# Kernel tuning notes

Measured on AMD Instinct MI355X. Metric: run time of the kernel, lower is better.

The kernel has to match this reference:

```python
import jax, jax.numpy as jnp
import numpy as np

B, FIELD, H_PREV, H_NEXT = 4096, 128, 128, 256


def setup_inputs() -> dict:
    key = jax.random.key(0)
    k0, k1, k2, k3 = jax.random.split(key, 4)
    x0 = jax.random.normal(k0, (B, FIELD), dtype=jnp.float32)
    x = jax.random.normal(k1, (B, H_PREV), dtype=jnp.float32)
    # Conv1d(1, H_NEXT, kernel=stride=H_PREV*FIELD) weight, reshaped so that
    # flat index k = f*H_PREV + p  ->  W[o, f, p]
    fan_in = H_PREV * FIELD
    bound = 1.0 / np.sqrt(fan_in)
    W = jax.random.uniform(k2, (H_NEXT, FIELD, H_PREV), dtype=jnp.float32, minval=-bound, maxval=bound)
    b = jax.random.uniform(k3, (H_NEXT,), dtype=jnp.float32, minval=-bound, maxval=bound)
    return {"x0": x0, "x": x, "W": W, "b": b}


def reference(x0, x, W, b):
    # outer product x0[b,f]*x[b,p] flattened then full-window conv == bilinear form
    outer = x0[:, :, None] * x[:, None, :]            # [B, FIELD, H_PREV]
    out = jnp.einsum('bfp,ofp->bo', outer, W) + b      # [B, H_NEXT]
    return out[:, :, None]                             # [B, H_NEXT, 1] like Conv1d output
```

## Files before the change

kernel.cpp:

```cpp
#include <hip/hip_runtime.h>


typedef _Float16 f16x8 __attribute__((ext_vector_type(8)));
typedef float    f32x4 __attribute__((ext_vector_type(4)));

#define WS_WT_OFF  0
#define WS_XF_OFF  8388608
#define WS_X0_OFF  9437184
#define WS_NEEDED  10485760

__device__ __forceinline__ void gl_lds16(const void* g, void* l) {
  __builtin_amdgcn_global_load_lds(
      (const __attribute__((address_space(1))) void*)g,
      (__attribute__((address_space(3))) void*)l, 16, 0, 0);
}

#define VMW(N) asm volatile("s_waitcnt vmcnt(" #N ")" ::: "memory")

__global__ __launch_bounds__(256) void prep_kernel(
    const float* __restrict__ x0, const float* __restrict__ x,
    const float* __restrict__ W, _Float16* __restrict__ WT2,
    _Float16* __restrict__ Xf, _Float16* __restrict__ X0T2)
{
  int i = blockIdx.x * 256 + threadIdx.x;
  if (i < 524288) {
    int o = i >> 11, k8 = i & 2047;
    const float* s = W + ((size_t)o << 14) + ((size_t)k8 << 3);
    f16x8 h;
#pragma unroll
    for (int e = 0; e < 8; ++e) h[e] = (_Float16)s[e];
    int ks = k8 >> 2, g = k8 & 3, ob = o >> 6, o6 = o & 63;
    int wv = ks >> 6, r = ks & 63, f = r >> 2, q = r & 3;
    int widx = q * 16 + f;
    *(f16x8*)(WT2 + ((size_t)((ob * 512 + wv * 64 + widx) * 4 + g)) * 512 +
              o6 * 8) = h;
  } else if (i < 589824) {
    int j = i - 524288;
    int r = j >> 4, seg = j & 15;
    const float* s = x + r * 128 + seg * 8;
    f16x8 h;
#pragma unroll
    for (int e = 0; e < 8; ++e) h[e] = (_Float16)s[e];
    int segp = seg ^ (r & 7);
    *(f16x8*)(Xf + r * 128 + segp * 8) = h;
  } else {
    int j = i - 589824;
    int mb = j >> 10, rem = j & 1023;
    int row = rem >> 4, jb = rem & 15;
    f16x8 h;
#pragma unroll
    for (int e = 0; e < 8; ++e)
      h[e] = (_Float16)x0[(size_t)(mb * 64 + row) * 128 + jb * 8 + e];
    *(f16x8*)(X0T2 + (size_t)mb * 8192 + row * 128 + (jb ^ (row & 7)) * 8) = h;
  }
}

__global__ __launch_bounds__(512, 2) void gemm_kernel(
    const _Float16* __restrict__ WT2, const _Float16* __restrict__ Xf,
    const _Float16* __restrict__ X0T2, const float* __restrict__ bias,
    float* __restrict__ out)
{
  __shared__ __align__(16) char smem[139264];

  const int bid = blockIdx.x;
  const int mb  = bid >> 2;
  const int ob  = bid & 3;

  const int t  = threadIdx.x;
  const int l  = t & 63;
  const int wv = t >> 6;
  const int lr = l & 15;
  const int lg = l >> 4;
  const int l16 = l * 16;
  const int swz = lr & 7;
  const int slotbase = wv * 12288;

  const char* wsrc = (const char*)WT2 + ((size_t)(ob * 512 + wv * 64)) * 4096;

  const char* xsb = (const char*)Xf + (size_t)mb * 16384;
  gl_lds16(xsb + 0 * 8192 + t * 16, smem + 98304 + 0 * 8192 + t * 16);
  gl_lds16(xsb + 1 * 8192 + t * 16, smem + 98304 + 1 * 8192 + t * 16);
  const char* x0b = (const char*)X0T2 + (size_t)mb * 16384;
  gl_lds16(x0b + 0 * 8192 + t * 16, smem + 114688 + 0 * 8192 + t * 16);
  gl_lds16(x0b + 1 * 8192 + t * 16, smem + 114688 + 1 * 8192 + t * 16);
#pragma unroll
  for (int w = 0; w < 3; ++w)
#pragma unroll
    for (int i = 0; i < 4; ++i)
      gl_lds16(wsrc + w * 4096 + i * 1024 + l16,
               smem + slotbase + w * 4096 + i * 1024 + l16);
  VMW(8);
  __builtin_amdgcn_s_barrier();

  f32x4 acc[4][4] = {};
  f16x8 xa[4], x0v[4], bwA[4], bwB[4];

#pragma unroll
  for (int m = 0; m < 4; ++m)
    xa[m] = *(const f16x8*)(smem + 98304 + (m * 16 + lr) * 256 +
                            (((0 * 4 + lg) ^ swz) << 4));
#pragma unroll
  for (int m = 0; m < 4; ++m)
    x0v[m] = *(const f16x8*)(smem + 114688 + (m * 16 + lr) * 256 +
                             (((wv * 2 + 0) ^ swz) << 4));
#pragma unroll
  for (int n = 0; n < 4; ++n)
    bwA[n] = *(const f16x8*)(smem + slotbase + 0 * 4096 + lg * 1024 +
                             (n * 16 + lr) * 16);

#define STEP(WI, BUFRD, BUFWR, STG, VMC) { \
    if (STG) { \
      _Pragma("unroll") \
      for (int i = 0; i < 4; ++i) \
        gl_lds16(wsrc + ((WI) + 3) * 4096 + i * 1024 + l16, \
                 smem + slotbase + ((WI) % 3) * 4096 + i * 1024 + l16); \
    } \
    VMW(VMC); \
    if ((WI) < 63) { \
      _Pragma("unroll") \
      for (int n = 0; n < 4; ++n) \
        BUFWR[n] = *(const f16x8*)(smem + slotbase + (((WI) + 1) % 3) * 4096 + \
                                   lg * 1024 + (n * 16 + lr) * 16); \
    } \
    f16x8 av[4]; \
    _Pragma("unroll") \
    for (int m = 0; m < 4; ++m) { \
      _Float16 sh = x0v[m][(WI) & 7]; \
      av[m] = xa[m] * sh; \
    } \
    if ((((WI) + 1) & 15) == 0 && (WI) < 63) { \
      _Pragma("unroll") \
      for (int m = 0; m < 4; ++m) \
        xa[m] = *(const f16x8*)(smem + 98304 + (m * 16 + lr) * 256 + \
                 ((((((WI) + 1) >> 4) * 4 + lg) ^ swz) << 4)); \
    } \
    if ((((WI) + 1) & 7) == 0 && (WI) < 63) { \
      _Pragma("unroll") \
      for (int m = 0; m < 4; ++m) \
        x0v[m] = *(const f16x8*)(smem + 114688 + (m * 16 + lr) * 256 + \
                  (((wv * 2 + ((((WI) + 1) >> 3) & 1)) ^ swz) << 4)); \
    } \
    _Pragma("unroll") \
    for (int m = 0; m < 4; ++m) { \
      _Pragma("unroll") \
      for (int n = 0; n < 4; ++n) \
        acc[m][n] = __builtin_amdgcn_mfma_f32_16x16x32_f16( \
            av[m], BUFRD[n], acc[m][n], 0, 0, 0); \
    } \
  }

#define SE(WI, STG, VMC) STEP(WI, bwA, bwB, STG, VMC)
#define SO(WI, STG, VMC) STEP(WI, bwB, bwA, STG, VMC)

  SE(0,1,8)  SO(1,1,8)  SE(2,1,8)  SO(3,1,8)  SE(4,1,8)  SO(5,1,8)
  SE(6,1,8)  SO(7,1,8)  SE(8,1,8)  SO(9,1,8)  SE(10,1,8) SO(11,1,8)
  SE(12,1,8) SO(13,1,8) SE(14,1,8) SO(15,1,8) SE(16,1,8) SO(17,1,8)
  SE(18,1,8) SO(19,1,8) SE(20,1,8) SO(21,1,8) SE(22,1,8) SO(23,1,8)
  SE(24,1,8) SO(25,1,8) SE(26,1,8) SO(27,1,8) SE(28,1,8) SO(29,1,8)
  SE(30,1,8) SO(31,1,8) SE(32,1,8) SO(33,1,8) SE(34,1,8) SO(35,1,8)
  SE(36,1,8) SO(37,1,8) SE(38,1,8) SO(39,1,8) SE(40,1,8) SO(41,1,8)
  SE(42,1,8) SO(43,1,8) SE(44,1,8) SO(45,1,8) SE(46,1,8) SO(47,1,8)
  SE(48,1,8) SO(49,1,8) SE(50,1,8) SO(51,1,8) SE(52,1,8) SO(53,1,8)
  SE(54,1,8) SO(55,1,8) SE(56,1,8) SO(57,1,8) SE(58,1,8) SO(59,1,8)
  SE(60,1,8) SO(61,0,4) SE(62,0,0) SO(63,0,0)

#undef SE
#undef SO
#undef STEP

  asm volatile("s_waitcnt vmcnt(0) lgkmcnt(0)" ::: "memory");
  __builtin_amdgcn_s_barrier();

#pragma unroll
  for (int m = 0; m < 4; ++m)
#pragma unroll
    for (int n = 0; n < 4; ++n)
      *(f32x4*)(smem + wv * 17408 + (n * 16 + lr) * 272 +
                (m * 16 + lg * 4) * 4) = acc[m][n];

  asm volatile("s_waitcnt lgkmcnt(0)" ::: "memory");
  __builtin_amdgcn_s_barrier();

  {
    const int row = t >> 3, c8 = (t & 7) * 8;
    float v[8];
#pragma unroll
    for (int c = 0; c < 8; ++c) {
      float s = 0.f;
#pragma unroll
      for (int w = 0; w < 8; ++w)
        s += *(const float*)(smem + w * 17408 + (c8 + c) * 272 + row * 4);
      v[c] = s;
    }
    const float4 b0 = *(const float4*)(bias + ob * 64 + c8);
    const float4 b1 = *(const float4*)(bias + ob * 64 + c8 + 4);
    float* op = out + (size_t)(mb * 64 + row) * 256 + ob * 64 + c8;
    float4 o0 = {v[0] + b0.x, v[1] + b0.y, v[2] + b0.z, v[3] + b0.w};
    float4 o1 = {v[4] + b1.x, v[5] + b1.y, v[6] + b1.z, v[7] + b1.w};
    *(float4*)(op)     = o0;
    *(float4*)(op + 4) = o1;
  }
}

__global__ __launch_bounds__(256) void naive_kernel(
    const float* __restrict__ x0, const float* __restrict__ x,
    const float* __restrict__ W, const float* __restrict__ bias,
    float* __restrict__ out)
{
  __shared__ float x0_s[16][128];
  __shared__ float x_s[16][128];
  const int tid = threadIdx.x;
  const int b0  = blockIdx.x * 16;
  for (int i = tid; i < 16 * 128; i += 256) {
    int bb = i >> 7, c = i & 127;
    x0_s[bb][c] = x0[(size_t)(b0 + bb) * 128 + c];
    x_s[bb][c]  = x[(size_t)(b0 + bb) * 128 + c];
  }
  __syncthreads();
  const int lane = tid & 63, wv = tid >> 6;
  for (int o = wv; o < 256; o += 4) {
    float acc[16];
#pragma unroll
    for (int bb = 0; bb < 16; ++bb) acc[bb] = 0.f;
    for (int it = 0; it < 256; ++it) {
      int k = it * 64 + lane;
      float wval = W[(size_t)o * 16384 + k];
      int f = k >> 7, p = k & 127;
#pragma unroll
      for (int bb = 0; bb < 16; ++bb)
        acc[bb] += wval * (x0_s[bb][f] * x_s[bb][p]);
    }
#pragma unroll
    for (int bb = 0; bb < 16; ++bb) {
      float v = acc[bb];
      for (int off = 32; off; off >>= 1) v += __shfl_down(v, off);
      if (lane == 0) out[(size_t)(b0 + bb) * 256 + o] = v + bias[o];
    }
  }
}

extern "C" void kernel_launch(void* const* d_in, const int* in_sizes, int n_in,
                              void* d_out, int out_size, void* d_ws,
                              size_t ws_size, hipStream_t stream)
{
  const float* x0   = (const float*)d_in[0];
  const float* x    = (const float*)d_in[1];
  const float* W    = (const float*)d_in[2];
  const float* bias = (const float*)d_in[3];
  float* out = (float*)d_out;

  if (ws_size >= (size_t)WS_NEEDED) {
    _Float16* WT2  = (_Float16*)((char*)d_ws + WS_WT_OFF);
    _Float16* Xf   = (_Float16*)((char*)d_ws + WS_XF_OFF);
    _Float16* X0T2 = (_Float16*)((char*)d_ws + WS_X0_OFF);
    prep_kernel<<<2560, 256, 0, stream>>>(x0, x, W, WT2, Xf, X0T2);
    gemm_kernel<<<256, 512, 0, stream>>>(WT2, Xf, X0T2, bias, out);
  } else {
    naive_kernel<<<256, 256, 0, stream>>>(x0, x, W, bias, out);
  }
}
```

Before: 49.41 us.

## Load GEMM weights directly into registers with triple buffering instead of LDS staging

Weight tiles were previously copied global→LDS with async global_load_lds and then read back into registers with manual vmcnt waits. Now each wave loads its weight fragments straight from global memory into three rotating register buffers, two steps ahead. The x and x0 tiles stay in LDS, now placed at the start of shared memory. This removes the LDS round trip and the LDS write and read traffic for weights. In exchange it adds register pressure and relies on compiler-inserted waits for global-load latency.

```diff
diff --git a/kernel.cpp b/kernel.cpp
--- a/kernel.cpp
+++ b/kernel.cpp
@@ -14,8 +14,6 @@
       (const __attribute__((address_space(1))) void*)g,
       (__attribute__((address_space(3))) void*)l, 16, 0, 0);
 }
-
-#define VMW(N) asm volatile("s_waitcnt vmcnt(" #N ")" ::: "memory")
 
 __global__ __launch_bounds__(256) void prep_kernel(
     const float* __restrict__ x0, const float* __restrict__ x,
@@ -71,73 +69,56 @@
   const int wv = t >> 6;
   const int lr = l & 15;
   const int lg = l >> 4;
-  const int l16 = l * 16;
   const int swz = lr & 7;
-  const int slotbase = wv * 12288;
 
   const char* wsrc = (const char*)WT2 + ((size_t)(ob * 512 + wv * 64)) * 4096;
+  const int wofs = lg * 1024 + lr * 16;
 
   const char* xsb = (const char*)Xf + (size_t)mb * 16384;
-  gl_lds16(xsb + 0 * 8192 + t * 16, smem + 98304 + 0 * 8192 + t * 16);
-  gl_lds16(xsb + 1 * 8192 + t * 16, smem + 98304 + 1 * 8192 + t * 16);
+  gl_lds16(xsb + 0 * 8192 + t * 16, smem + 0 * 8192 + t * 16);
+  gl_lds16(xsb + 1 * 8192 + t * 16, smem + 1 * 8192 + t * 16);
   const char* x0b = (const char*)X0T2 + (size_t)mb * 16384;
-  gl_lds16(x0b + 0 * 8192 + t * 16, smem + 114688 + 0 * 8192 + t * 16);
-  gl_lds16(x0b + 1 * 8192 + t * 16, smem + 114688 + 1 * 8192 + t * 16);
-#pragma unroll
-  for (int w = 0; w < 3; ++w)
-#pragma unroll
-    for (int i = 0; i < 4; ++i)
-      gl_lds16(wsrc + w * 4096 + i * 1024 + l16,
-               smem + slotbase + w * 4096 + i * 1024 + l16);
-  VMW(8);
-  __builtin_amdgcn_s_barrier();
+  gl_lds16(x0b + 0 * 8192 + t * 16, smem + 16384 + 0 * 8192 + t * 16);
+  gl_lds16(x0b + 1 * 8192 + t * 16, smem + 16384 + 1 * 8192 + t * 16);
+  __syncthreads();
 
   f32x4 acc[4][4] = {};
-  f16x8 xa[4], x0v[4], bwA[4], bwB[4];
+  f16x8 xa[4], x0v[4], bw0[4], bw1[4], bw2[4];
 
 #pragma unroll
   for (int m = 0; m < 4; ++m)
-    xa[m] = *(const f16x8*)(smem + 98304 + (m * 16 + lr) * 256 +
-                            (((0 * 4 + lg) ^ swz) << 4));
+    xa[m] = *(const f16x8*)(smem + (m * 16 + lr) * 256 + ((lg ^ swz) << 4));
 #pragma unroll
   for (int m = 0; m < 4; ++m)
-    x0v[m] = *(const f16x8*)(smem + 114688 + (m * 16 + lr) * 256 +
-                             (((wv * 2 + 0) ^ swz) << 4));
-#pragma unroll
-  for (int n = 0; n < 4; ++n)
-    bwA[n] = *(const f16x8*)(smem + slotbase + 0 * 4096 + lg * 1024 +
-                             (n * 16 + lr) * 16);
-
-#define STEP(WI, BUFRD, BUFWR, STG, VMC) { \
+    x0v[m] = *(const f16x8*)(smem + 16384 + (m * 16 + lr) * 256 +
+                             (((wv * 2) ^ swz) << 4));
+#pragma unroll
+  for (int i = 0; i < 4; ++i)
+    bw0[i] = *(const f16x8*)(wsrc + 0 * 4096 + i * 256 + wofs);
+#pragma unroll
+  for (int i = 0; i < 4; ++i)
+    bw1[i] = *(const f16x8*)(wsrc + 1 * 4096 + i * 256 + wofs);
+
+#define STEP(WI, BR, BW_, STG) { \
     if (STG) { \
       _Pragma("unroll") \
       for (int i = 0; i < 4; ++i) \
-        gl_lds16(wsrc + ((WI) + 3) * 4096 + i * 1024 + l16, \
-                 smem + slotbase + ((WI) % 3) * 4096 + i * 1024 + l16); \
-    } \
-    VMW(VMC); \
-    if ((WI) < 63) { \
-      _Pragma("unroll") \
-      for (int n = 0; n < 4; ++n) \
-        BUFWR[n] = *(const f16x8*)(smem + slotbase + (((WI) + 1) % 3) * 4096 + \
-                                   lg * 1024 + (n * 16 + lr) * 16); \
+        BW_[i] = *(const f16x8*)(wsrc + ((WI) + 2) * 4096 + i * 256 + wofs); \
     } \
     f16x8 av[4]; \
     _Pragma("unroll") \
-    for (int m = 0; m < 4; ++m) { \
-      _Float16 sh = x0v[m][(WI) & 7]; \
-      av[m] = xa[m] * sh; \
-    } \
+    for (int m = 0; m < 4; ++m) \
+      av[m] = xa[m] * x0v[m][(WI) & 7]; \
     if ((((WI) + 1) & 15) == 0 && (WI) < 63) { \
       _Pragma("unroll") \
       for (int m = 0; m < 4; ++m) \
-        xa[m] = *(const f16x8*)(smem + 98304 + (m * 16 + lr) * 256 + \
+        xa[m] = *(const f16x8*)(smem + (m * 16 + lr) * 256 + \
                  ((((((WI) + 1) >> 4) * 4 + lg) ^ swz) << 4)); \
     } \
     if ((((WI) + 1) & 7) == 0 && (WI) < 63) { \
       _Pragma("unroll") \
       for (int m = 0; m < 4; ++m) \
-        x0v[m] = *(const f16x8*)(smem + 114688 + (m * 16 + lr) * 256 + \
+        x0v[m] = *(const f16x8*)(smem + 16384 + (m * 16 + lr) * 256 + \
                   (((wv * 2 + ((((WI) + 1) >> 3) & 1)) ^ swz) << 4)); \
     } \
     _Pragma("unroll") \
@@ -145,31 +126,32 @@
       _Pragma("unroll") \
       for (int n = 0; n < 4; ++n) \
         acc[m][n] = __builtin_amdgcn_mfma_f32_16x16x32_f16( \
-            av[m], BUFRD[n], acc[m][n], 0, 0, 0); \
-    } \
-  }
-
-#define SE(WI, STG, VMC) STEP(WI, bwA, bwB, STG, VMC)
-#define SO(WI, STG, VMC) STEP(WI, bwB, bwA, STG, VMC)
-
-  SE(0,1,8)  SO(1,1,8)  SE(2,1,8)  SO(3,1,8)  SE(4,1,8)  SO(5,1,8)
-  SE(6,1,8)  SO(7,1,8)  SE(8,1,8)  SO(9,1,8)  SE(10,1,8) SO(11,1,8)
-  SE(12,1,8) SO(13,1,8) SE(14,1,8) SO(15,1,8) SE(16,1,8) SO(17,1,8)
-  SE(18,1,8) SO(19,1,8) SE(20,1,8) SO(21,1,8) SE(22,1,8) SO(23,1,8)
-  SE(24,1,8) SO(25,1,8) SE(26,1,8) SO(27,1,8) SE(28,1,8) SO(29,1,8)
-  SE(30,1,8) SO(31,1,8) SE(32,1,8) SO(33,1,8) SE(34,1,8) SO(35,1,8)
-  SE(36,1,8) SO(37,1,8) SE(38,1,8) SO(39,1,8) SE(40,1,8) SO(41,1,8)
-  SE(42,1,8) SO(43,1,8) SE(44,1,8) SO(45,1,8) SE(46,1,8) SO(47,1,8)
-  SE(48,1,8) SO(49,1,8) SE(50,1,8) SO(51,1,8) SE(52,1,8) SO(53,1,8)
-  SE(54,1,8) SO(55,1,8) SE(56,1,8) SO(57,1,8) SE(58,1,8) SO(59,1,8)
-  SE(60,1,8) SO(61,0,4) SE(62,0,0) SO(63,0,0)
-
-#undef SE
-#undef SO
+            av[m], BR[n], acc[m][n], 0, 0, 0); \
+    } \
+  }
+
+#define S0(WI, STG) STEP(WI, bw0, bw2, STG)
+#define S1(WI, STG) STEP(WI, bw1, bw0, STG)
+#define S2(WI, STG) STEP(WI, bw2, bw1, STG)
+
+  S0(0,1)  S1(1,1)  S2(2,1)  S0(3,1)  S1(4,1)  S2(5,1)
+  S0(6,1)  S1(7,1)  S2(8,1)  S0(9,1)  S1(10,1) S2(11,1)
+  S0(12,1) S1(13,1) S2(14,1) S0(15,1) S1(16,1) S2(17,1)
+  S0(18,1) S1(19,1) S2(20,1) S0(21,1) S1(22,1) S2(23,1)
+  S0(24,1) S1(25,1) S2(26,1) S0(27,1) S1(28,1) S2(29,1)
+  S0(30,1) S1(31,1) S2(32,1) S0(33,1) S1(34,1) S2(35,1)
+  S0(36,1) S1(37,1) S2(38,1) S0(39,1) S1(40,1) S2(41,1)
+  S0(42,1) S1(43,1) S2(44,1) S0(45,1) S1(46,1) S2(47,1)
+  S0(48,1) S1(49,1) S2(50,1) S0(51,1) S1(52,1) S2(53,1)
+  S0(54,1) S1(55,1) S2(56,1) S0(57,1) S1(58,1) S2(59,1)
+  S0(60,1) S1(61,1) S2(62,0) S0(63,0)
+
+#undef S0
+#undef S1
+#undef S2
 #undef STEP
 
-  asm volatile("s_waitcnt vmcnt(0) lgkmcnt(0)" ::: "memory");
-  __builtin_amdgcn_s_barrier();
+  __syncthreads();
 
 #pragma unroll
   for (int m = 0; m < 4; ++m)
@@ -178,8 +160,7 @@
       *(f32x4*)(smem + wv * 17408 + (n * 16 + lr) * 272 +
                 (m * 16 + lg * 4) * 4) = acc[m][n];
 
-  asm volatile("s_waitcnt lgkmcnt(0)" ::: "memory");
-  __builtin_amdgcn_s_barrier();
+  __syncthreads();
 
   {
     const int row = t >> 3, c8 = (t & 7) * 8;
```

Measured after the change: 49.16 us (median of 2 runs). Within noise of the previous version (-0.5%).
